# Kernel tuning notes

Measured on AMD Instinct MI355X. Metric: run time of the kernel, lower is better.

The kernel has to match this reference:

```python
import jax, jax.numpy as jnp
import numpy as np

B, P, E, H, L = 16, 500, 128, 8, 3
N = P + 1
HD = E // H
LEAKY = 0.2
LN_EPS = 1e-5


def setup_inputs() -> dict:
    key = jax.random.key(0)
    ks = jax.random.split(key, 12)
    depot_xy = jax.random.uniform(ks[0], (B, 1, 2), dtype=jnp.float32)
    node_xy_demand_TW = jax.random.uniform(ks[1], (B, P, 5), dtype=jnp.float32)
    # random adjacency with guaranteed self-loops (avoids all -inf softmax rows)
    adj = jax.random.uniform(ks[2], (B, N, N)) > 0.5
    adj_mask = adj | jnp.eye(N, dtype=bool)[None]
    # embedding layers (nn.Linear: y = x @ W^T + b; we store W as (in, out))
    dep_W = jax.random.normal(ks[3], (2, E), dtype=jnp.float32) * 0.1
    dep_b = jnp.zeros((E,), dtype=jnp.float32)
    node_W = jax.random.normal(ks[4], (5, E), dtype=jnp.float32) * 0.1
    node_b = jnp.zeros((E,), dtype=jnp.float32)
    # per-layer GAT params, stacked over L
    W = jax.random.normal(ks[5], (L, E, E), dtype=jnp.float32) * (1.0 / np.sqrt(E))
    attn = jax.random.normal(ks[6], (L, H, 2 * HD), dtype=jnp.float32) * 0.1
    ln_g = jnp.ones((L, E), dtype=jnp.float32)
    ln_b = jnp.zeros((L, E), dtype=jnp.float32)
    return dict(depot_xy=depot_xy, node_xy_demand_TW=node_xy_demand_TW,
                adj_mask=adj_mask, dep_W=dep_W, dep_b=dep_b,
                node_W=node_W, node_b=node_b, W=W, attn=attn,
                ln_g=ln_g, ln_b=ln_b)


def _layernorm(x, g, b):
    mu = jnp.mean(x, axis=-1, keepdims=True)
    var = jnp.var(x, axis=-1, keepdims=True)
    return (x - mu) * jax.lax.rsqrt(var + LN_EPS) * g + b


def _gat_layer(x, adj_mask, Wl, attn_l, g, b):
    # x: (B,N,E)
    xW = x @ Wl                                   # (B,N,E)
    xWh = xW.reshape(B, N, H, HD)
    a1, a2 = attn_l[:, :HD], attn_l[:, HD:]       # (H,HD) each
    # concat-score factorization: e_ij = <a1, xW_i> + <a2, xW_j>
    ei = jnp.einsum('bnhd,hd->bnh', xWh, a1)      # (B,N,H)
    ej = jnp.einsum('bnhd,hd->bnh', xWh, a2)
    e = ei[:, :, None, :] + ej[:, None, :, :]     # (B,N,N,H)
    e = jnp.where(e >= 0, e, LEAKY * e)           # LeakyReLU
    e = jnp.where(adj_mask[..., None], e, -jnp.inf)
    alpha = jax.nn.softmax(e, axis=2)             # over source nodes j
    out = jnp.einsum('bijh,bjhd->bihd', alpha, xWh).reshape(B, N, E)
    out = _layernorm(out + xW, g, b)
    return jax.nn.elu(out)


def reference(depot_xy, node_xy_demand_TW, adj_mask, dep_W, dep_b,
              node_W, node_b, W, attn, ln_g, ln_b):
    depot_emb = depot_xy @ dep_W + dep_b          # (B,1,E)
    node_emb = node_xy_demand_TW @ node_W + node_b  # (B,P,E)
    x = jnp.concatenate([depot_emb, node_emb], axis=1)  # (B,N,E)
    for l in range(L):
        x = _gat_layer(x, adj_mask, W[l], attn[l], ln_g[l], ln_b[l])
    return x
```

## Files before the change

kernel.cpp:

```cpp
#include <hip/hip_runtime.h>
#include <hip/hip_bf16.h>
#include <math.h>

#define Bn 16
#define Pn 500
#define Nn 501
#define En 128
#define Hn 8
#define HDn 16
#define Ln 3
#define ROWS (Bn*Nn)
#define LN_EPS 1e-5f

typedef __attribute__((ext_vector_type(8))) short bf16x8;
typedef __attribute__((ext_vector_type(4))) float f32x4;

__device__ inline short f2bf(float x) {
  __hip_bfloat16 h = __float2bfloat16(x);
  return *reinterpret_cast<short*>(&h);
}
__device__ inline float bf2f(short s) {
  __hip_bfloat16 h = *reinterpret_cast<__hip_bfloat16*>(&s);
  return __bfloat162float(h);
}

__global__ __launch_bounds__(256) void embed_kernel(
    const float* __restrict__ depot, const float* __restrict__ node,
    const float* __restrict__ depW, const float* __restrict__ depB,
    const float* __restrict__ nodeW, const float* __restrict__ nodeB,
    float* __restrict__ x) {
  int idx = blockIdx.x * 256 + threadIdx.x;
  if (idx >= ROWS * En) return;
  int row = idx / En, e = idx % En;
  int b = row / Nn, n = row % Nn;
  float v;
  if (n == 0) {
    v = depB[e] + depot[b * 2 + 0] * depW[0 * En + e]
                + depot[b * 2 + 1] * depW[1 * En + e];
  } else {
    const float* np_ = node + (b * Pn + (n - 1)) * 5;
    v = nodeB[e];
#pragma unroll
    for (int k = 0; k < 5; k++) v += np_[k] * nodeW[k * En + e];
  }
  x[idx] = v;
}

__global__ __launch_bounds__(512) void adjpack_kernel(
    const int* __restrict__ adj, unsigned* __restrict__ bits) {
  int blk = blockIdx.x;
  int b = blk >> 9, i = blk & 511;
  int gi = (i < Nn) ? i : (Nn - 1);
  int t = threadIdx.x;
  int v = (t < Nn) ? adj[((size_t)b * Nn + gi) * Nn + t] : 0;
  unsigned long long mask = __ballot(v != 0);
  int wave = t >> 6;
  if ((t & 63) == 0) {
    unsigned* wp = bits + ((size_t)b * 512 + i) * 16 + wave * 2;
    wp[0] = (unsigned)(mask & 0xffffffffull);
    wp[1] = (unsigned)(mask >> 32);
  }
}

__global__ __launch_bounds__(256) void gemm_xw(
    const float* __restrict__ x, const float* __restrict__ Wl,
    float* __restrict__ xw) {
  __shared__ float As[64][33];
  __shared__ float Bs[32][128];
  int tid = threadIdx.x;
  int row0 = blockIdx.x * 64;
  int tc = tid % 32;
  int trg = tid / 32;
  float acc[8][4];
#pragma unroll
  for (int m = 0; m < 8; m++)
#pragma unroll
    for (int n = 0; n < 4; n++) acc[m][n] = 0.f;

  for (int k0 = 0; k0 < 128; k0 += 32) {
#pragma unroll
    for (int s = 0; s < 8; s++) {
      int a = tid + s * 256;
      int r = a >> 5, c = a & 31;
      int gr = row0 + r;
      As[r][c] = (gr < ROWS) ? x[gr * 128 + k0 + c] : 0.f;
    }
#pragma unroll
    for (int s = 0; s < 16; s++) {
      int a2 = tid + s * 256;
      int r = a2 >> 7, c = a2 & 127;
      Bs[r][c] = Wl[(k0 + r) * 128 + c];
    }
    __syncthreads();
#pragma unroll
    for (int kk = 0; kk < 32; kk++) {
      float bv[4];
#pragma unroll
      for (int n = 0; n < 4; n++) bv[n] = Bs[kk][tc * 4 + n];
#pragma unroll
      for (int m = 0; m < 8; m++) {
        float av = As[trg * 8 + m][kk];
#pragma unroll
        for (int n = 0; n < 4; n++) acc[m][n] += av * bv[n];
      }
    }
    __syncthreads();
  }
#pragma unroll
  for (int m = 0; m < 8; m++) {
    int gr = row0 + trg * 8 + m;
    if (gr < ROWS) {
#pragma unroll
      for (int n = 0; n < 4; n++) xw[gr * 128 + tc * 4 + n] = acc[m][n];
    }
  }
}

__global__ __launch_bounds__(256) void eij_kernel(
    const float* __restrict__ xw, const float* __restrict__ attn_l,
    float* __restrict__ ei, float* __restrict__ ej) {
  int idx = blockIdx.x * 256 + threadIdx.x;
  if (idx >= ROWS * Hn) return;
  int row = idx >> 3, h = idx & 7;
  const float* xr = xw + row * 128 + h * 16;
  const float* a1 = attn_l + h * 32;
  const float* a2 = a1 + 16;
  float s1 = 0.f, s2 = 0.f;
#pragma unroll
  for (int d = 0; d < 16; d++) {
    float v = xr[d];
    s1 += v * a1[d];
    s2 += v * a2[d];
  }
  ei[idx] = s1;
  ej[idx] = s2;
}

__global__ __launch_bounds__(512) void attn_fused(
    const float* __restrict__ xw, const float* __restrict__ ei,
    const float* __restrict__ ej, const unsigned* __restrict__ adjbits,
    const float* __restrict__ g, const float* __restrict__ bb,
    float* __restrict__ dst) {
  __shared__ float ejl[Hn][516];
  __shared__ float Vt[64][132];
  __shared__ unsigned adjw[32][17];
  __shared__ float oout[32][132];

  int blk = blockIdx.x;
  int b = blk >> 4;
  int i0 = (blk & 15) << 5;
  int t = threadIdx.x;
  int h = t >> 6;
  int lane = t & 63;
  int li = lane & 15;
  int lg = lane >> 4;

  for (int s = t; s < 512 * Hn; s += 512) {
    int j = s >> 3, hh = s & 7;
    ejl[hh][j] = (j < Nn) ? ej[((size_t)b * Nn + j) * Hn + hh] : 0.f;
  }
  for (int s = t; s < 32 * 16; s += 512) {
    int r = s >> 4, w = s & 15;
    int gi = i0 + r; if (gi >= Nn) gi = Nn - 1;
    adjw[r][w] = adjbits[((size_t)b * 512 + gi) * 16 + w];
  }

  int gi0 = i0 + li;      if (gi0 >= Nn) gi0 = Nn - 1;
  int gi1 = i0 + 16 + li; if (gi1 >= Nn) gi1 = Nn - 1;
  float eiv0 = ei[((size_t)b * Nn + gi0) * Hn + h];
  float eiv1 = ei[((size_t)b * Nn + gi1) * Hn + h];

  f32x4 acc0 = {0.f, 0.f, 0.f, 0.f};
  f32x4 acc1 = {0.f, 0.f, 0.f, 0.f};
  float m0 = -1e30f, m1 = -1e30f, l0 = 0.f, l1 = 0.f;

  for (int jt = 0; jt < 8; ++jt) {
    int j0 = jt << 6;
    __syncthreads();
    for (int s = t; s < 64 * 32; s += 512) {
      int jj = s >> 5, c4 = (s & 31) << 2;
      int gj = j0 + jj;
      float4 v;
      if (gj < Nn) v = *(const float4*)&xw[((size_t)b * Nn + gj) * En + c4];
      else         v = make_float4(0.f, 0.f, 0.f, 0.f);
      *(float4*)&Vt[jj][c4] = v;
    }
    __syncthreads();

    float sc0[2][8], sc1[2][8];
#pragma unroll
    for (int kw = 0; kw < 2; ++kw) {
      const float* pj = &ejl[h][j0 + (kw << 5) + (lg << 3)];
      unsigned mb0 = (adjw[li][(j0 >> 5) + kw] >> (lg << 3)) & 0xffu;
      unsigned mb1 = (adjw[16 + li][(j0 >> 5) + kw] >> (lg << 3)) & 0xffu;
#pragma unroll
      for (int e = 0; e < 8; ++e) {
        float ejv = pj[e];
        float s0 = eiv0 + ejv; s0 = fmaxf(s0, 0.2f * s0);
        float s1 = eiv1 + ejv; s1 = fmaxf(s1, 0.2f * s1);
        sc0[kw][e] = ((mb0 >> e) & 1u) ? s0 : -INFINITY;
        sc1[kw][e] = ((mb1 >> e) & 1u) ? s1 : -INFINITY;
      }
    }
    float tm0 = -INFINITY, tm1 = -INFINITY;
#pragma unroll
    for (int kw = 0; kw < 2; ++kw)
#pragma unroll
      for (int e = 0; e < 8; ++e) {
        tm0 = fmaxf(tm0, sc0[kw][e]);
        tm1 = fmaxf(tm1, sc1[kw][e]);
      }
    tm0 = fmaxf(tm0, __shfl_xor(tm0, 16)); tm0 = fmaxf(tm0, __shfl_xor(tm0, 32));
    tm1 = fmaxf(tm1, __shfl_xor(tm1, 16)); tm1 = fmaxf(tm1, __shfl_xor(tm1, 32));
    float mn0 = fmaxf(m0, tm0), mn1 = fmaxf(m1, tm1);
    float fr0 = __expf(m0 - mn0), fr1 = __expf(m1 - mn1);
    m0 = mn0; m1 = mn1;

    float ts0 = 0.f, ts1 = 0.f;
    short ph0[2][8], pl0[2][8], ph1[2][8], pl1[2][8];
#pragma unroll
    for (int kw = 0; kw < 2; ++kw)
#pragma unroll
      for (int e = 0; e < 8; ++e) {
        float p0 = __expf(sc0[kw][e] - mn0);
        float p1 = __expf(sc1[kw][e] - mn1);
        ts0 += p0; ts1 += p1;
        short h0 = f2bf(p0); ph0[kw][e] = h0; pl0[kw][e] = f2bf(p0 - bf2f(h0));
        short h1 = f2bf(p1); ph1[kw][e] = h1; pl1[kw][e] = f2bf(p1 - bf2f(h1));
      }
    ts0 += __shfl_xor(ts0, 16); ts0 += __shfl_xor(ts0, 32);
    ts1 += __shfl_xor(ts1, 16); ts1 += __shfl_xor(ts1, 32);
    l0 = l0 * fr0 + ts0;
    l1 = l1 * fr1 + ts1;

    int base = lg << 2;
#pragma unroll
    for (int r = 0; r < 4; ++r) {
      acc0[r] *= __shfl(fr0, base + r);
      acc1[r] *= __shfl(fr1, base + r);
    }

#pragma unroll
    for (int kw = 0; kw < 2; ++kw) {
      short vh[8], vl[8];
#pragma unroll
      for (int e = 0; e < 8; ++e) {
        float v = Vt[(kw << 5) + (lg << 3) + e][h * 16 + li];
        short hv = f2bf(v); vh[e] = hv; vl[e] = f2bf(v - bf2f(hv));
      }
      bf16x8 vbh = {vh[0], vh[1], vh[2], vh[3], vh[4], vh[5], vh[6], vh[7]};
      bf16x8 vbl = {vl[0], vl[1], vl[2], vl[3], vl[4], vl[5], vl[6], vl[7]};
      bf16x8 pah0 = {ph0[kw][0], ph0[kw][1], ph0[kw][2], ph0[kw][3],
                     ph0[kw][4], ph0[kw][5], ph0[kw][6], ph0[kw][7]};
      bf16x8 pal0 = {pl0[kw][0], pl0[kw][1], pl0[kw][2], pl0[kw][3],
                     pl0[kw][4], pl0[kw][5], pl0[kw][6], pl0[kw][7]};
      bf16x8 pah1 = {ph1[kw][0], ph1[kw][1], ph1[kw][2], ph1[kw][3],
                     ph1[kw][4], ph1[kw][5], ph1[kw][6], ph1[kw][7]};
      bf16x8 pal1 = {pl1[kw][0], pl1[kw][1], pl1[kw][2], pl1[kw][3],
                     pl1[kw][4], pl1[kw][5], pl1[kw][6], pl1[kw][7]};
      acc0 = __builtin_amdgcn_mfma_f32_16x16x32_bf16(pah0, vbh, acc0, 0, 0, 0);
      acc0 = __builtin_amdgcn_mfma_f32_16x16x32_bf16(pah0, vbl, acc0, 0, 0, 0);
      acc0 = __builtin_amdgcn_mfma_f32_16x16x32_bf16(pal0, vbh, acc0, 0, 0, 0);
      acc1 = __builtin_amdgcn_mfma_f32_16x16x32_bf16(pah1, vbh, acc1, 0, 0, 0);
      acc1 = __builtin_amdgcn_mfma_f32_16x16x32_bf16(pah1, vbl, acc1, 0, 0, 0);
      acc1 = __builtin_amdgcn_mfma_f32_16x16x32_bf16(pal1, vbh, acc1, 0, 0, 0);
    }
  }

  {
    int base = lg << 2;
#pragma unroll
    for (int r = 0; r < 4; ++r) {
      float d0 = __shfl(l0, base + r);
      float d1 = __shfl(l1, base + r);
      oout[base + r][h * 16 + li] = acc0[r] / d0;
      oout[16 + base + r][h * 16 + li] = acc1[r] / d1;
    }
  }
  __syncthreads();

  {
    int row = t >> 4;
    int c0 = (t & 15) << 3;
    int gi = i0 + row;
    bool valid = gi < Nn;
    int gic = valid ? gi : Nn - 1;
    const float* xr = &xw[((size_t)b * Nn + gic) * En + c0];
    float4 o1 = *(float4*)&oout[row][c0];
    float4 o2 = *(float4*)&oout[row][c0 + 4];
    float4 x1 = *(const float4*)xr;
    float4 x2 = *(const float4*)(xr + 4);
    float y[8];
    y[0] = o1.x + x1.x; y[1] = o1.y + x1.y; y[2] = o1.z + x1.z; y[3] = o1.w + x1.w;
    y[4] = o2.x + x2.x; y[5] = o2.y + x2.y; y[6] = o2.z + x2.z; y[7] = o2.w + x2.w;
    float sum = 0.f, sq = 0.f;
#pragma unroll
    for (int u = 0; u < 8; ++u) { sum += y[u]; sq += y[u] * y[u]; }
#pragma unroll
    for (int mk = 1; mk <= 8; mk <<= 1) {
      sum += __shfl_xor(sum, mk);
      sq  += __shfl_xor(sq, mk);
    }
    float mu = sum * (1.f / 128.f);
    float var = sq * (1.f / 128.f) - mu * mu;
    float rs = rsqrtf(var + LN_EPS);
    if (valid) {
      const float4 g1 = *(const float4*)&g[c0];
      const float4 g2 = *(const float4*)&g[c0 + 4];
      const float4 b1 = *(const float4*)&bb[c0];
      const float4 b2 = *(const float4*)&bb[c0 + 4];
      float gv[8] = {g1.x, g1.y, g1.z, g1.w, g2.x, g2.y, g2.z, g2.w};
      float bv[8] = {b1.x, b1.y, b1.z, b1.w, b2.x, b2.y, b2.z, b2.w};
      float* op = &dst[((size_t)b * Nn + gi) * En + c0];
      float zo[8];
#pragma unroll
      for (int u = 0; u < 8; ++u) {
        float z = (y[u] - mu) * rs * gv[u] + bv[u];
        zo[u] = (z > 0.f) ? z : expm1f(z);
      }
      *(float4*)op = make_float4(zo[0], zo[1], zo[2], zo[3]);
      *(float4*)(op + 4) = make_float4(zo[4], zo[5], zo[6], zo[7]);
    }
  }
}

extern "C" void kernel_launch(void* const* d_in, const int* in_sizes, int n_in,
                              void* d_out, int out_size, void* d_ws, size_t ws_size,
                              hipStream_t stream) {
  const float* depot = (const float*)d_in[0];
  const float* node  = (const float*)d_in[1];
  const int*   adj   = (const int*)d_in[2];
  const float* depW  = (const float*)d_in[3];
  const float* depB  = (const float*)d_in[4];
  const float* nodeW = (const float*)d_in[5];
  const float* nodeB = (const float*)d_in[6];
  const float* W     = (const float*)d_in[7];
  const float* attn  = (const float*)d_in[8];
  const float* lng   = (const float*)d_in[9];
  const float* lnb   = (const float*)d_in[10];
  float* out = (float*)d_out;

  float* xa = (float*)d_ws;
  float* xw = xa + (size_t)ROWS * En;
  float* ei = xw + (size_t)ROWS * En;
  float* ej = ei + (size_t)ROWS * Hn;
  unsigned* adjbits = (unsigned*)(ej + (size_t)ROWS * Hn);

  adjpack_kernel<<<Bn * 512, 512, 0, stream>>>(adj, adjbits);
  embed_kernel<<<(ROWS * En + 255) / 256, 256, 0, stream>>>(
      depot, node, depW, depB, nodeW, nodeB, xa);

  for (int l = 0; l < Ln; l++) {
    gemm_xw<<<(ROWS + 63) / 64, 256, 0, stream>>>(xa, W + (size_t)l * En * En, xw);
    eij_kernel<<<(ROWS * Hn + 255) / 256, 256, 0, stream>>>(
        xw, attn + (size_t)l * Hn * 2 * HDn, ei, ej);
    float* dst = (l == Ln - 1) ? out : xa;
    attn_fused<<<Bn * 16, 512, 0, stream>>>(
        xw, ei, ej, adjbits, lng + (size_t)l * En, lnb + (size_t)l * En, dst);
  }
}
```

Measured before the change: 259.2 us.

## Fuse all stages into a single cooperative persistent kernel with grid syncs

Replaces the eleven separate launches (adjacency packing, embedding, and per-layer GEMM, score and attention kernels) with one cooperative kernel of 256 blocks that uses grid-wide barriers between phases. The GEMM and the e_i/e_j projection are fused so the scores come from a shared-memory tile, and one shared-memory union serves both phases. The aim is to remove launch overhead and the global round trip of the separate score kernel. In exchange, the GEMM and adjacency-packing phases run on only 256 blocks of 512 threads, and each grid sync adds a barrier cost.

```diff
diff --git a/kernel.cpp b/kernel.cpp
--- a/kernel.cpp
+++ b/kernel.cpp
@@ -1,13 +1,15 @@
 #include <hip/hip_runtime.h>
+#include <hip/hip_cooperative_groups.h>
 #include <hip/hip_bf16.h>
 #include <math.h>
+
+namespace cg = cooperative_groups;
 
 #define Bn 16
 #define Pn 500
 #define Nn 501
 #define En 128
 #define Hn 8
-#define HDn 16
 #define Ln 3
 #define ROWS (Bn*Nn)
 #define LN_EPS 1e-5f
@@ -24,303 +26,315 @@
   return __bfloat162float(h);
 }
 
-__global__ __launch_bounds__(256) void embed_kernel(
+struct SmemGemm {
+  float Bs[32][128];
+  float As[32][33];
+  float xt[32][132];
+};
+struct SmemAttn {
+  float ejl[Hn][516];
+  float Vt[64][132];
+  unsigned adjw[32][17];
+  float oout[32][132];
+};
+union Smem { SmemGemm g; SmemAttn a; };
+
+__global__ __launch_bounds__(512) void mega_kernel(
     const float* __restrict__ depot, const float* __restrict__ node,
+    const int* __restrict__ adj,
     const float* __restrict__ depW, const float* __restrict__ depB,
     const float* __restrict__ nodeW, const float* __restrict__ nodeB,
-    float* __restrict__ x) {
-  int idx = blockIdx.x * 256 + threadIdx.x;
-  if (idx >= ROWS * En) return;
-  int row = idx / En, e = idx % En;
-  int b = row / Nn, n = row % Nn;
-  float v;
-  if (n == 0) {
-    v = depB[e] + depot[b * 2 + 0] * depW[0 * En + e]
-                + depot[b * 2 + 1] * depW[1 * En + e];
-  } else {
-    const float* np_ = node + (b * Pn + (n - 1)) * 5;
-    v = nodeB[e];
-#pragma unroll
-    for (int k = 0; k < 5; k++) v += np_[k] * nodeW[k * En + e];
-  }
-  x[idx] = v;
-}
-
-__global__ __launch_bounds__(512) void adjpack_kernel(
-    const int* __restrict__ adj, unsigned* __restrict__ bits) {
-  int blk = blockIdx.x;
-  int b = blk >> 9, i = blk & 511;
-  int gi = (i < Nn) ? i : (Nn - 1);
-  int t = threadIdx.x;
-  int v = (t < Nn) ? adj[((size_t)b * Nn + gi) * Nn + t] : 0;
-  unsigned long long mask = __ballot(v != 0);
-  int wave = t >> 6;
-  if ((t & 63) == 0) {
-    unsigned* wp = bits + ((size_t)b * 512 + i) * 16 + wave * 2;
-    wp[0] = (unsigned)(mask & 0xffffffffull);
-    wp[1] = (unsigned)(mask >> 32);
-  }
-}
-
-__global__ __launch_bounds__(256) void gemm_xw(
-    const float* __restrict__ x, const float* __restrict__ Wl,
-    float* __restrict__ xw) {
-  __shared__ float As[64][33];
-  __shared__ float Bs[32][128];
-  int tid = threadIdx.x;
-  int row0 = blockIdx.x * 64;
-  int tc = tid % 32;
-  int trg = tid / 32;
-  float acc[8][4];
-#pragma unroll
-  for (int m = 0; m < 8; m++)
-#pragma unroll
-    for (int n = 0; n < 4; n++) acc[m][n] = 0.f;
-
-  for (int k0 = 0; k0 < 128; k0 += 32) {
-#pragma unroll
-    for (int s = 0; s < 8; s++) {
-      int a = tid + s * 256;
-      int r = a >> 5, c = a & 31;
-      int gr = row0 + r;
-      As[r][c] = (gr < ROWS) ? x[gr * 128 + k0 + c] : 0.f;
-    }
-#pragma unroll
-    for (int s = 0; s < 16; s++) {
-      int a2 = tid + s * 256;
-      int r = a2 >> 7, c = a2 & 127;
-      Bs[r][c] = Wl[(k0 + r) * 128 + c];
-    }
-    __syncthreads();
-#pragma unroll
-    for (int kk = 0; kk < 32; kk++) {
-      float bv[4];
-#pragma unroll
-      for (int n = 0; n < 4; n++) bv[n] = Bs[kk][tc * 4 + n];
-#pragma unroll
-      for (int m = 0; m < 8; m++) {
-        float av = As[trg * 8 + m][kk];
-#pragma unroll
-        for (int n = 0; n < 4; n++) acc[m][n] += av * bv[n];
-      }
-    }
-    __syncthreads();
-  }
-#pragma unroll
-  for (int m = 0; m < 8; m++) {
-    int gr = row0 + trg * 8 + m;
-    if (gr < ROWS) {
-#pragma unroll
-      for (int n = 0; n < 4; n++) xw[gr * 128 + tc * 4 + n] = acc[m][n];
+    const float* __restrict__ W, const float* __restrict__ attnw,
+    const float* __restrict__ lng, const float* __restrict__ lnb,
+    float* __restrict__ out,
+    float* __restrict__ xa, float* __restrict__ xw,
+    float* __restrict__ ei, float* __restrict__ ej,
+    unsigned* __restrict__ adjbits) {
+  cg::grid_group gg = cg::this_grid();
+  __shared__ Smem sm;
+  const int blk = blockIdx.x;
+  const int t = threadIdx.x;
+
+  {
+    int lanebit = t & 63, wave = t >> 6;
+    for (int r = 0; r < 32; ++r) {
+      int row = blk * 32 + r;
+      if (row >= ROWS) break;
+      int v = (t < Nn) ? adj[(size_t)row * Nn + t] : 0;
+      unsigned long long mask = __ballot(v != 0);
+      if (lanebit == 0) {
+        int b = row / Nn, i = row - b * Nn;
+        unsigned* wp = adjbits + ((size_t)(b * 512 + i)) * 16 + wave * 2;
+        wp[0] = (unsigned)(mask & 0xffffffffull);
+        wp[1] = (unsigned)(mask >> 32);
+      }
     }
   }
-}
-
-__global__ __launch_bounds__(256) void eij_kernel(
-    const float* __restrict__ xw, const float* __restrict__ attn_l,
-    float* __restrict__ ei, float* __restrict__ ej) {
-  int idx = blockIdx.x * 256 + threadIdx.x;
-  if (idx >= ROWS * Hn) return;
-  int row = idx >> 3, h = idx & 7;
-  const float* xr = xw + row * 128 + h * 16;
-  const float* a1 = attn_l + h * 32;
-  const float* a2 = a1 + 16;
-  float s1 = 0.f, s2 = 0.f;
-#pragma unroll
-  for (int d = 0; d < 16; d++) {
-    float v = xr[d];
-    s1 += v * a1[d];
-    s2 += v * a2[d];
-  }
-  ei[idx] = s1;
-  ej[idx] = s2;
-}
-
-__global__ __launch_bounds__(512) void attn_fused(
-    const float* __restrict__ xw, const float* __restrict__ ei,
-    const float* __restrict__ ej, const unsigned* __restrict__ adjbits,
-    const float* __restrict__ g, const float* __restrict__ bb,
-    float* __restrict__ dst) {
-  __shared__ float ejl[Hn][516];
-  __shared__ float Vt[64][132];
-  __shared__ unsigned adjw[32][17];
-  __shared__ float oout[32][132];
-
-  int blk = blockIdx.x;
-  int b = blk >> 4;
-  int i0 = (blk & 15) << 5;
-  int t = threadIdx.x;
-  int h = t >> 6;
-  int lane = t & 63;
-  int li = lane & 15;
-  int lg = lane >> 4;
-
-  for (int s = t; s < 512 * Hn; s += 512) {
-    int j = s >> 3, hh = s & 7;
-    ejl[hh][j] = (j < Nn) ? ej[((size_t)b * Nn + j) * Hn + hh] : 0.f;
-  }
-  for (int s = t; s < 32 * 16; s += 512) {
-    int r = s >> 4, w = s & 15;
-    int gi = i0 + r; if (gi >= Nn) gi = Nn - 1;
-    adjw[r][w] = adjbits[((size_t)b * 512 + gi) * 16 + w];
-  }
-
-  int gi0 = i0 + li;      if (gi0 >= Nn) gi0 = Nn - 1;
-  int gi1 = i0 + 16 + li; if (gi1 >= Nn) gi1 = Nn - 1;
-  float eiv0 = ei[((size_t)b * Nn + gi0) * Hn + h];
-  float eiv1 = ei[((size_t)b * Nn + gi1) * Hn + h];
-
-  f32x4 acc0 = {0.f, 0.f, 0.f, 0.f};
-  f32x4 acc1 = {0.f, 0.f, 0.f, 0.f};
-  float m0 = -1e30f, m1 = -1e30f, l0 = 0.f, l1 = 0.f;
-
-  for (int jt = 0; jt < 8; ++jt) {
-    int j0 = jt << 6;
-    __syncthreads();
-    for (int s = t; s < 64 * 32; s += 512) {
-      int jj = s >> 5, c4 = (s & 31) << 2;
-      int gj = j0 + jj;
-      float4 v;
-      if (gj < Nn) v = *(const float4*)&xw[((size_t)b * Nn + gj) * En + c4];
-      else         v = make_float4(0.f, 0.f, 0.f, 0.f);
-      *(float4*)&Vt[jj][c4] = v;
-    }
-    __syncthreads();
-
-    float sc0[2][8], sc1[2][8];
-#pragma unroll
-    for (int kw = 0; kw < 2; ++kw) {
-      const float* pj = &ejl[h][j0 + (kw << 5) + (lg << 3)];
-      unsigned mb0 = (adjw[li][(j0 >> 5) + kw] >> (lg << 3)) & 0xffu;
-      unsigned mb1 = (adjw[16 + li][(j0 >> 5) + kw] >> (lg << 3)) & 0xffu;
-#pragma unroll
-      for (int e = 0; e < 8; ++e) {
-        float ejv = pj[e];
-        float s0 = eiv0 + ejv; s0 = fmaxf(s0, 0.2f * s0);
-        float s1 = eiv1 + ejv; s1 = fmaxf(s1, 0.2f * s1);
-        sc0[kw][e] = ((mb0 >> e) & 1u) ? s0 : -INFINITY;
-        sc1[kw][e] = ((mb1 >> e) & 1u) ? s1 : -INFINITY;
-      }
-    }
-    float tm0 = -INFINITY, tm1 = -INFINITY;
-#pragma unroll
-    for (int kw = 0; kw < 2; ++kw)
-#pragma unroll
-      for (int e = 0; e < 8; ++e) {
-        tm0 = fmaxf(tm0, sc0[kw][e]);
-        tm1 = fmaxf(tm1, sc1[kw][e]);
-      }
-    tm0 = fmaxf(tm0, __shfl_xor(tm0, 16)); tm0 = fmaxf(tm0, __shfl_xor(tm0, 32));
-    tm1 = fmaxf(tm1, __shfl_xor(tm1, 16)); tm1 = fmaxf(tm1, __shfl_xor(tm1, 32));
-    float mn0 = fmaxf(m0, tm0), mn1 = fmaxf(m1, tm1);
-    float fr0 = __expf(m0 - mn0), fr1 = __expf(m1 - mn1);
-    m0 = mn0; m1 = mn1;
-
-    float ts0 = 0.f, ts1 = 0.f;
-    short ph0[2][8], pl0[2][8], ph1[2][8], pl1[2][8];
-#pragma unroll
-    for (int kw = 0; kw < 2; ++kw)
-#pragma unroll
-      for (int e = 0; e < 8; ++e) {
-        float p0 = __expf(sc0[kw][e] - mn0);
-        float p1 = __expf(sc1[kw][e] - mn1);
-        ts0 += p0; ts1 += p1;
-        short h0 = f2bf(p0); ph0[kw][e] = h0; pl0[kw][e] = f2bf(p0 - bf2f(h0));
-        short h1 = f2bf(p1); ph1[kw][e] = h1; pl1[kw][e] = f2bf(p1 - bf2f(h1));
-      }
-    ts0 += __shfl_xor(ts0, 16); ts0 += __shfl_xor(ts0, 32);
-    ts1 += __shfl_xor(ts1, 16); ts1 += __shfl_xor(ts1, 32);
-    l0 = l0 * fr0 + ts0;
-    l1 = l1 * fr1 + ts1;
-
-    int base = lg << 2;
-#pragma unroll
-    for (int r = 0; r < 4; ++r) {
-      acc0[r] *= __shfl(fr0, base + r);
-      acc1[r] *= __shfl(fr1, base + r);
-    }
-
-#pragma unroll
-    for (int kw = 0; kw < 2; ++kw) {
-      short vh[8], vl[8];
-#pragma unroll
-      for (int e = 0; e < 8; ++e) {
-        float v = Vt[(kw << 5) + (lg << 3) + e][h * 16 + li];
-        short hv = f2bf(v); vh[e] = hv; vl[e] = f2bf(v - bf2f(hv));
-      }
-      bf16x8 vbh = {vh[0], vh[1], vh[2], vh[3], vh[4], vh[5], vh[6], vh[7]};
-      bf16x8 vbl = {vl[0], vl[1], vl[2], vl[3], vl[4], vl[5], vl[6], vl[7]};
-      bf16x8 pah0 = {ph0[kw][0], ph0[kw][1], ph0[kw][2], ph0[kw][3],
-                     ph0[kw][4], ph0[kw][5], ph0[kw][6], ph0[kw][7]};
-      bf16x8 pal0 = {pl0[kw][0], pl0[kw][1], pl0[kw][2], pl0[kw][3],
-                     pl0[kw][4], pl0[kw][5], pl0[kw][6], pl0[kw][7]};
-      bf16x8 pah1 = {ph1[kw][0], ph1[kw][1], ph1[kw][2], ph1[kw][3],
-                     ph1[kw][4], ph1[kw][5], ph1[kw][6], ph1[kw][7]};
-      bf16x8 pal1 = {pl1[kw][0], pl1[kw][1], pl1[kw][2], pl1[kw][3],
-                     pl1[kw][4], pl1[kw][5], pl1[kw][6], pl1[kw][7]};
-      acc0 = __builtin_amdgcn_mfma_f32_16x16x32_bf16(pah0, vbh, acc0, 0, 0, 0);
-      acc0 = __builtin_amdgcn_mfma_f32_16x16x32_bf16(pah0, vbl, acc0, 0, 0, 0);
-      acc0 = __builtin_amdgcn_mfma_f32_16x16x32_bf16(pal0, vbh, acc0, 0, 0, 0);
-      acc1 = __builtin_amdgcn_mfma_f32_16x16x32_bf16(pah1, vbh, acc1, 0, 0, 0);
-      acc1 = __builtin_amdgcn_mfma_f32_16x16x32_bf16(pah1, vbl, acc1, 0, 0, 0);
-      acc1 = __builtin_amdgcn_mfma_f32_16x16x32_bf16(pal1, vbh, acc1, 0, 0, 0);
+  {
+#pragma unroll
+    for (int s = 0; s < 8; ++s) {
+      int idx = (blk * 512 + t) + s * 131072;
+      if (idx < ROWS * En) {
+        int row = idx >> 7, e = idx & 127;
+        int b = row / Nn, n = row - b * Nn;
+        float v;
+        if (n == 0) {
+          v = depB[e] + depot[b * 2 + 0] * depW[0 * En + e]
+                      + depot[b * 2 + 1] * depW[1 * En + e];
+        } else {
+          const float* np_ = node + ((size_t)b * Pn + (n - 1)) * 5;
+          v = nodeB[e];
+#pragma unroll
+          for (int k = 0; k < 5; k++) v += np_[k] * nodeW[k * En + e];
+        }
+        xa[idx] = v;
+      }
     }
   }
-
-  {
-    int base = lg << 2;
-#pragma unroll
-    for (int r = 0; r < 4; ++r) {
-      float d0 = __shfl(l0, base + r);
-      float d1 = __shfl(l1, base + r);
-      oout[base + r][h * 16 + li] = acc0[r] / d0;
-      oout[16 + base + r][h * 16 + li] = acc1[r] / d1;
+  gg.sync();
+
+  for (int l = 0; l < Ln; ++l) {
+    const float* Wl = W + (size_t)l * En * En;
+    const float* al = attnw + (size_t)l * Hn * 32;
+    const float* g  = lng + (size_t)l * En;
+    const float* bb = lnb + (size_t)l * En;
+    float* dst = (l == Ln - 1) ? out : xa;
+
+    {
+      int row0 = blk * 32;
+      if (row0 < ROWS) {
+        int tc = t & 31, tr = t >> 5;
+        float acc[2][4] = {{0.f,0.f,0.f,0.f},{0.f,0.f,0.f,0.f}};
+        for (int k0 = 0; k0 < 128; k0 += 32) {
+          {
+            int r0 = t >> 5, c0 = t & 31;
+            int gr = row0 + r0;
+            sm.g.As[r0][c0] = (gr < ROWS) ? xa[(size_t)gr * 128 + k0 + c0] : 0.f;
+            int s1 = t + 512;
+            int r1 = s1 >> 5, c1 = s1 & 31;
+            gr = row0 + r1;
+            sm.g.As[r1][c1] = (gr < ROWS) ? xa[(size_t)gr * 128 + k0 + c1] : 0.f;
+          }
+#pragma unroll
+          for (int s = 0; s < 8; ++s) {
+            int a2 = t + s * 512, r = a2 >> 7, c = a2 & 127;
+            sm.g.Bs[r][c] = Wl[(k0 + r) * 128 + c];
+          }
+          __syncthreads();
+#pragma unroll
+          for (int kk = 0; kk < 32; ++kk) {
+            float4 bv = *(float4*)&sm.g.Bs[kk][tc * 4];
+            float av0 = sm.g.As[tr * 2][kk];
+            float av1 = sm.g.As[tr * 2 + 1][kk];
+            acc[0][0] += av0 * bv.x; acc[0][1] += av0 * bv.y;
+            acc[0][2] += av0 * bv.z; acc[0][3] += av0 * bv.w;
+            acc[1][0] += av1 * bv.x; acc[1][1] += av1 * bv.y;
+            acc[1][2] += av1 * bv.z; acc[1][3] += av1 * bv.w;
+          }
+          __syncthreads();
+        }
+#pragma unroll
+        for (int m = 0; m < 2; ++m) {
+          int lr = tr * 2 + m;
+          int gr = row0 + lr;
+          float4 vv = make_float4(acc[m][0], acc[m][1], acc[m][2], acc[m][3]);
+          *(float4*)&sm.g.xt[lr][tc * 4] = vv;
+          if (gr < ROWS) *(float4*)&xw[(size_t)gr * 128 + tc * 4] = vv;
+        }
+        __syncthreads();
+        {
+          int r = t >> 4, rest = t & 15;
+          int h = rest >> 1, sel = rest & 1;
+          int gr = row0 + r;
+          if (gr < ROWS) {
+            const float* av = al + h * 32 + sel * 16;
+            float ssum = 0.f;
+#pragma unroll
+            for (int d = 0; d < 16; ++d) ssum += sm.g.xt[r][h * 16 + d] * av[d];
+            (sel ? ej : ei)[(size_t)gr * 8 + h] = ssum;
+          }
+        }
+      }
     }
-  }
-  __syncthreads();
-
-  {
-    int row = t >> 4;
-    int c0 = (t & 15) << 3;
-    int gi = i0 + row;
-    bool valid = gi < Nn;
-    int gic = valid ? gi : Nn - 1;
-    const float* xr = &xw[((size_t)b * Nn + gic) * En + c0];
-    float4 o1 = *(float4*)&oout[row][c0];
-    float4 o2 = *(float4*)&oout[row][c0 + 4];
-    float4 x1 = *(const float4*)xr;
-    float4 x2 = *(const float4*)(xr + 4);
-    float y[8];
-    y[0] = o1.x + x1.x; y[1] = o1.y + x1.y; y[2] = o1.z + x1.z; y[3] = o1.w + x1.w;
-    y[4] = o2.x + x2.x; y[5] = o2.y + x2.y; y[6] = o2.z + x2.z; y[7] = o2.w + x2.w;
-    float sum = 0.f, sq = 0.f;
-#pragma unroll
-    for (int u = 0; u < 8; ++u) { sum += y[u]; sq += y[u] * y[u]; }
-#pragma unroll
-    for (int mk = 1; mk <= 8; mk <<= 1) {
-      sum += __shfl_xor(sum, mk);
-      sq  += __shfl_xor(sq, mk);
+    gg.sync();
+
+    {
+      int b = blk >> 4;
+      int i0 = (blk & 15) << 5;
+      int h = t >> 6;
+      int lane = t & 63;
+      int li = lane & 15;
+      int lg = lane >> 4;
+
+      for (int s = t; s < 512 * Hn; s += 512) {
+        int j = s >> 3, hh = s & 7;
+        sm.a.ejl[hh][j] = (j < Nn) ? ej[((size_t)b * Nn + j) * Hn + hh] : 0.f;
+      }
+      for (int s = t; s < 32 * 16; s += 512) {
+        int r = s >> 4, w = s & 15;
+        int gi = i0 + r; if (gi >= Nn) gi = Nn - 1;
+        sm.a.adjw[r][w] = adjbits[((size_t)b * 512 + gi) * 16 + w];
+      }
+
+      int gi0 = i0 + li;      if (gi0 >= Nn) gi0 = Nn - 1;
+      int gi1 = i0 + 16 + li; if (gi1 >= Nn) gi1 = Nn - 1;
+      float eiv0 = ei[((size_t)b * Nn + gi0) * Hn + h];
+      float eiv1 = ei[((size_t)b * Nn + gi1) * Hn + h];
+
+      f32x4 acc0 = {0.f, 0.f, 0.f, 0.f};
+      f32x4 acc1 = {0.f, 0.f, 0.f, 0.f};
+      float m0 = -1e30f, m1 = -1e30f, l0 = 0.f, l1 = 0.f;
+
+      for (int jt = 0; jt < 8; ++jt) {
+        int j0 = jt << 6;
+        __syncthreads();
+        for (int s = t; s < 64 * 32; s += 512) {
+          int jj = s >> 5, c4 = (s & 31) << 2;
+          int gj = j0 + jj;
+          float4 v;
+          if (gj < Nn) v = *(const float4*)&xw[((size_t)b * Nn + gj) * En + c4];
+          else         v = make_float4(0.f, 0.f, 0.f, 0.f);
+          *(float4*)&sm.a.Vt[jj][c4] = v;
+        }
+        __syncthreads();
+
+        float sc0[2][8], sc1[2][8];
+#pragma unroll
+        for (int kw = 0; kw < 2; ++kw) {
+          const float* pj = &sm.a.ejl[h][j0 + (kw << 5) + (lg << 3)];
+          unsigned mb0 = (sm.a.adjw[li][(j0 >> 5) + kw] >> (lg << 3)) & 0xffu;
+          unsigned mb1 = (sm.a.adjw[16 + li][(j0 >> 5) + kw] >> (lg << 3)) & 0xffu;
+#pragma unroll
+          for (int e = 0; e < 8; ++e) {
+            float ejv = pj[e];
+            float s0 = eiv0 + ejv; s0 = fmaxf(s0, 0.2f * s0);
+            float s1 = eiv1 + ejv; s1 = fmaxf(s1, 0.2f * s1);
+            sc0[kw][e] = ((mb0 >> e) & 1u) ? s0 : -INFINITY;
+            sc1[kw][e] = ((mb1 >> e) & 1u) ? s1 : -INFINITY;
+          }
+        }
+        float tm0 = -INFINITY, tm1 = -INFINITY;
+#pragma unroll
+        for (int kw = 0; kw < 2; ++kw)
+#pragma unroll
+          for (int e = 0; e < 8; ++e) {
+            tm0 = fmaxf(tm0, sc0[kw][e]);
+            tm1 = fmaxf(tm1, sc1[kw][e]);
+          }
+        tm0 = fmaxf(tm0, __shfl_xor(tm0, 16)); tm0 = fmaxf(tm0, __shfl_xor(tm0, 32));
+        tm1 = fmaxf(tm1, __shfl_xor(tm1, 16)); tm1 = fmaxf(tm1, __shfl_xor(tm1, 32));
+        float mn0 = fmaxf(m0, tm0), mn1 = fmaxf(m1, tm1);
+        float fr0 = __expf(m0 - mn0), fr1 = __expf(m1 - mn1);
+        m0 = mn0; m1 = mn1;
+
+        float ts0 = 0.f, ts1 = 0.f;
+        short ph0[2][8], pl0[2][8], ph1[2][8], pl1[2][8];
+#pragma unroll
+        for (int kw = 0; kw < 2; ++kw)
+#pragma unroll
+          for (int e = 0; e < 8; ++e) {
+            float p0 = __expf(sc0[kw][e] - mn0);
+            float p1 = __expf(sc1[kw][e] - mn1);
+            ts0 += p0; ts1 += p1;
+            short h0 = f2bf(p0); ph0[kw][e] = h0; pl0[kw][e] = f2bf(p0 - bf2f(h0));
+            short h1 = f2bf(p1); ph1[kw][e] = h1; pl1[kw][e] = f2bf(p1 - bf2f(h1));
+          }
+        ts0 += __shfl_xor(ts0, 16); ts0 += __shfl_xor(ts0, 32);
+        ts1 += __shfl_xor(ts1, 16); ts1 += __shfl_xor(ts1, 32);
+        l0 = l0 * fr0 + ts0;
+        l1 = l1 * fr1 + ts1;
+
+        int base = lg << 2;
+#pragma unroll
+        for (int r = 0; r < 4; ++r) {
+          acc0[r] *= __shfl(fr0, base + r);
+          acc1[r] *= __shfl(fr1, base + r);
+        }
+
+#pragma unroll
+        for (int kw = 0; kw < 2; ++kw) {
+          short vh[8], vl[8];
+#pragma unroll
+          for (int e = 0; e < 8; ++e) {
+            float v = sm.a.Vt[(kw << 5) + (lg << 3) + e][h * 16 + li];
+            short hv = f2bf(v); vh[e] = hv; vl[e] = f2bf(v - bf2f(hv));
+          }
+          bf16x8 vbh = {vh[0], vh[1], vh[2], vh[3], vh[4], vh[5], vh[6], vh[7]};
+          bf16x8 vbl = {vl[0], vl[1], vl[2], vl[3], vl[4], vl[5], vl[6], vl[7]};
+          bf16x8 pah0 = {ph0[kw][0], ph0[kw][1], ph0[kw][2], ph0[kw][3],
+                         ph0[kw][4], ph0[kw][5], ph0[kw][6], ph0[kw][7]};
+          bf16x8 pal0 = {pl0[kw][0], pl0[kw][1], pl0[kw][2], pl0[kw][3],
+                         pl0[kw][4], pl0[kw][5], pl0[kw][6], pl0[kw][7]};
+          bf16x8 pah1 = {ph1[kw][0], ph1[kw][1], ph1[kw][2], ph1[kw][3],
+                         ph1[kw][4], ph1[kw][5], ph1[kw][6], ph1[kw][7]};
+          bf16x8 pal1 = {pl1[kw][0], pl1[kw][1], pl1[kw][2], pl1[kw][3],
+                         pl1[kw][4], pl1[kw][5], pl1[kw][6], pl1[kw][7]};
+          acc0 = __builtin_amdgcn_mfma_f32_16x16x32_bf16(pah0, vbh, acc0, 0, 0, 0);
+          acc0 = __builtin_amdgcn_mfma_f32_16x16x32_bf16(pah0, vbl, acc0, 0, 0, 0);
+          acc0 = __builtin_amdgcn_mfma_f32_16x16x32_bf16(pal0, vbh, acc0, 0, 0, 0);
+          acc1 = __builtin_amdgcn_mfma_f32_16x16x32_bf16(pah1, vbh, acc1, 0, 0, 0);
+          acc1 = __builtin_amdgcn_mfma_f32_16x16x32_bf16(pah1, vbl, acc1, 0, 0, 0);
+          acc1 = __builtin_amdgcn_mfma_f32_16x16x32_bf16(pal1, vbh, acc1, 0, 0, 0);
+        }
+      }
+
+      {
+        int base = lg << 2;
+#pragma unroll
+        for (int r = 0; r < 4; ++r) {
+          float d0 = __shfl(l0, base + r);
+          float d1 = __shfl(l1, base + r);
+          sm.a.oout[base + r][h * 16 + li] = acc0[r] / d0;
+          sm.a.oout[16 + base + r][h * 16 + li] = acc1[r] / d1;
+        }
+      }
+      __syncthreads();
+
+      {
+        int row = t >> 4;
+        int c0 = (t & 15) << 3;
+        int gi = i0 + row;
+        bool valid = gi < Nn;
+        int gic = valid ? gi : Nn - 1;
+        const float* xr = &xw[((size_t)b * Nn + gic) * En + c0];
+        float4 o1 = *(float4*)&sm.a.oout[row][c0];
+        float4 o2 = *(float4*)&sm.a.oout[row][c0 + 4];
+        float4 x1 = *(const float4*)xr;
+        float4 x2 = *(const float4*)(xr + 4);
+        float y[8];
+        y[0] = o1.x + x1.x; y[1] = o1.y + x1.y; y[2] = o1.z + x1.z; y[3] = o1.w + x1.w;
+        y[4] = o2.x + x2.x; y[5] = o2.y + x2.y; y[6] = o2.z + x2.z; y[7] = o2.w + x2.w;
+        float sum = 0.f, sq = 0.f;
+#pragma unroll
+        for (int u = 0; u < 8; ++u) { sum += y[u]; sq += y[u] * y[u]; }
+#pragma unroll
+        for (int mk = 1; mk <= 8; mk <<= 1) {
+          sum += __shfl_xor(sum, mk);
+          sq  += __shfl_xor(sq, mk);
+        }
+        float mu = sum * (1.f / 128.f);
+        float var = sq * (1.f / 128.f) - mu * mu;
+        float rs = rsqrtf(var + LN_EPS);
+        if (valid) {
+          const float4 g1 = *(const float4*)&g[c0];
+          const float4 g2 = *(const float4*)&g[c0 + 4];
+          const float4 b1 = *(const float4*)&bb[c0];
+          const float4 b2 = *(const float4*)&bb[c0 + 4];
+          float gv[8] = {g1.x, g1.y, g1.z, g1.w, g2.x, g2.y, g2.z, g2.w};
+          float bv[8] = {b1.x, b1.y, b1.z, b1.w, b2.x, b2.y, b2.z, b2.w};
+          float* op = &dst[((size_t)b * Nn + gi) * En + c0];
+          float zo[8];
+#pragma unroll
+          for (int u = 0; u < 8; ++u) {
+            float z = (y[u] - mu) * rs * gv[u] + bv[u];
+            zo[u] = (z > 0.f) ? z : expm1f(z);
+          }
+          *(float4*)op = make_float4(zo[0], zo[1], zo[2], zo[3]);
+          *(float4*)(op + 4) = make_float4(zo[4], zo[5], zo[6], zo[7]);
+        }
+      }
     }
-    float mu = sum * (1.f / 128.f);
-    float var = sq * (1.f / 128.f) - mu * mu;
-    float rs = rsqrtf(var + LN_EPS);
-    if (valid) {
-      const float4 g1 = *(const float4*)&g[c0];
-      const float4 g2 = *(const float4*)&g[c0 + 4];
-      const float4 b1 = *(const float4*)&bb[c0];
-      const float4 b2 = *(const float4*)&bb[c0 + 4];
-      float gv[8] = {g1.x, g1.y, g1.z, g1.w, g2.x, g2.y, g2.z, g2.w};
-      float bv[8] = {b1.x, b1.y, b1.z, b1.w, b2.x, b2.y, b2.z, b2.w};
-      float* op = &dst[((size_t)b * Nn + gi) * En + c0];
-      float zo[8];
-#pragma unroll
-      for (int u = 0; u < 8; ++u) {
-        float z = (y[u] - mu) * rs * gv[u] + bv[u];
-        zo[u] = (z > 0.f) ? z : expm1f(z);
-      }
-      *(float4*)op = make_float4(zo[0], zo[1], zo[2], zo[3]);
-      *(float4*)(op + 4) = make_float4(zo[4], zo[5], zo[6], zo[7]);
-    }
+    if (l < Ln - 1) gg.sync();
   }
 }
 
@@ -335,7 +349,7 @@
   const float* nodeW = (const float*)d_in[5];
   const float* nodeB = (const float*)d_in[6];
   const float* W     = (const float*)d_in[7];
-  const float* attn  = (const float*)d_in[8];
+  const float* attnw = (const float*)d_in[8];
   const float* lng   = (const float*)d_in[9];
   const float* lnb   = (const float*)d_in[10];
   float* out = (float*)d_out;
@@ -346,16 +360,13 @@
   float* ej = ei + (size_t)ROWS * Hn;
   unsigned* adjbits = (unsigned*)(ej + (size_t)ROWS * Hn);
 
-  adjpack_kernel<<<Bn * 512, 512, 0, stream>>>(adj, adjbits);
-  embed_kernel<<<(ROWS * En + 255) / 256, 256, 0, stream>>>(
-      depot, node, depW, depB, nodeW, nodeB, xa);
-
-  for (int l = 0; l < Ln; l++) {
-    gemm_xw<<<(ROWS + 63) / 64, 256, 0, stream>>>(xa, W + (size_t)l * En * En, xw);
-    eij_kernel<<<(ROWS * Hn + 255) / 256, 256, 0, stream>>>(
-        xw, attn + (size_t)l * Hn * 2 * HDn, ei, ej);
-    float* dst = (l == Ln - 1) ? out : xa;
-    attn_fused<<<Bn * 16, 512, 0, stream>>>(
-        xw, ei, ej, adjbits, lng + (size_t)l * En, lnb + (size_t)l * En, dst);
-  }
+  void* args[] = {
+    (void*)&depot, (void*)&node, (void*)&adj,
+    (void*)&depW, (void*)&depB, (void*)&nodeW, (void*)&nodeB,
+    (void*)&W, (void*)&attnw, (void*)&lng, (void*)&lnb,
+    (void*)&out, (void*)&xa, (void*)&xw, (void*)&ei, (void*)&ej,
+    (void*)&adjbits
+  };
+  hipLaunchCooperativeKernel((const void*)mega_kernel, dim3(256), dim3(512),
+                             args, 0, stream);
 }
```

Result: slower. 465.0 us (+79.4%).
